# Kernel optimization log

Hardware: AMD Instinct MI355X
Metric: run time of the kernel (lower is better)

The kernel has to match this reference:

```python
import jax, jax.numpy as jnp
from jax import lax
import numpy as np

B, C, T = 128, 9, 512
M = 64                 # fourier modes
D_OB = 40
D_MODEL = C * D_OB     # 360
D_PE = 16
D = D_MODEL + D_PE     # 376
NHEAD = 4
DH = D // NHEAD        # 94
NHID = 2 * D_MODEL     # 720
NLAYERS = 3
FRAC = 0.5
MAX_PE = 100.0
EPS = 1e-5

def setup_inputs() -> dict:
    key = jax.random.key(0)
    ks = jax.random.split(key, 16)
    scale = 1.0 / (C * C)
    f32 = jnp.float32
    return {
        "x": jax.random.normal(ks[0], (B, C, T), f32),
        "w1r": scale * jax.random.uniform(ks[1], (C, C, M), f32),
        "w1i": scale * jax.random.uniform(ks[2], (C, C, M), f32),
        "conv_w": 0.1 * jax.random.normal(ks[3], (1, C, 3), f32),
        "bnf_g": jnp.ones((2 * M,), f32), "bnf_b": jnp.zeros((2 * M,), f32),
        "R_u": 1.0 + 0.02 * jax.random.normal(ks[4], (D_MODEL,), f32),
        "Wg1": 0.1 * jax.random.normal(ks[5], (D_OB, D_OB), f32),
        "Wg2": 0.1 * jax.random.normal(ks[6], (D_OB, D_OB), f32),
        "Wqkv": 0.02 * jax.random.normal(ks[7], (NLAYERS, D, 3 * D), f32),
        "bqkv": jnp.zeros((NLAYERS, 3 * D), f32),
        "Wo": 0.02 * jax.random.normal(ks[8], (NLAYERS, D, D), f32),
        "bo": jnp.zeros((NLAYERS, D), f32),
        "ln1g": jnp.ones((NLAYERS, D), f32), "ln1b": jnp.zeros((NLAYERS, D), f32),
        "W1": 0.02 * jax.random.normal(ks[9], (NLAYERS, D, NHID), f32),
        "b1": jnp.zeros((NLAYERS, NHID), f32),
        "W2": 0.02 * jax.random.normal(ks[10], (NLAYERS, NHID, D), f32),
        "b2": jnp.zeros((NLAYERS, D), f32),
        "ln2g": jnp.ones((NLAYERS, D), f32), "ln2b": jnp.zeros((NLAYERS, D), f32),
        "Wp": 0.02 * jax.random.normal(ks[11], (D, T), f32),
        "bp": jnp.zeros((T,), f32),
        "bnp_g": jnp.ones((T,), f32), "bnp_b": jnp.zeros((T,), f32),
    }

def _layernorm(z, g, b):
    m = z.mean(-1, keepdims=True)
    v = ((z - m) ** 2).mean(-1, keepdims=True)
    return (z - m) * lax.rsqrt(v + EPS) * g + b

def _batchnorm(z, g, b):  # training-mode BN over batch dim, z: [N, F]
    m = z.mean(0)
    v = ((z - m) ** 2).mean(0)
    return (z - m) * lax.rsqrt(v + EPS) * g + b

def _forward(x, w1r, w1i, conv_w, bnf_g, bnf_b, R_u, Wg1, Wg2,
             Wqkv, bqkv, Wo, bo, ln1g, ln1b, W1, b1, W2, b2, ln2g, ln2b,
             Wp, bp, bnp_g, bnp_b):
    # ---- SpectralConv1d (FrFT branch) ----
    xc = jnp.cos(x)                                   # [B,C,T]
    k = jnp.arange(T, dtype=jnp.float32)
    chirp = jnp.exp(-1j * jnp.pi * FRAC * k * k / T)  # FrFT chirp
    x_frft = jnp.fft.ifft(jnp.fft.fft(xc) * chirp)    # [B,C,T] complex
    w1 = (w1r + 1j * w1i).astype(jnp.complex64)
    out_modes = jnp.einsum('bix,iox->box', x_frft[:, :, :M], w1)   # [B,C,M]
    out_ft = jnp.concatenate([out_modes, jnp.zeros((B, C, T - M), jnp.complex64)], -1)
    ef = jnp.concatenate([jnp.abs(out_modes), jnp.angle(out_modes)], -1)  # [B,C,2M]
    # avg: Conv1d(C->1, k=3, pad=1, stride=1, no bias), then squeeze
    ef = lax.conv_general_dilated(ef, conv_w, window_strides=(1,), padding=((1, 1),),
                                  dimension_numbers=('NCH', 'OIH', 'NCH'))[:, 0, :]  # [B,2M]
    ef = jax.nn.relu(_batchnorm(ef, bnf_g, bnf_b))
    # ---- Raindrop branch ----
    src = jnp.transpose(x, (2, 0, 1))                 # [T,B,C]
    h = jnp.repeat(src, D_OB, axis=-1)                # repeat_interleave -> [T,B,d_model]
    h = jax.nn.relu(h * R_u)
    h4 = h.reshape(T, B, C, D_OB)
    adj = jnp.full((C, C), 1.0 / C, x.dtype)          # global_structure = ones, normalized
    h4 = jax.nn.relu(jnp.einsum('mn,tbnd,de->tbme', adj, h4, Wg1))
    h4 = jax.nn.relu(jnp.einsum('mn,tbnd,de->tbme', adj, h4, Wg2))
    h = h4.reshape(T, B, D_MODEL)
    # time positional encoding (PositionalEncodingTF, d_pe=16, MAX=100)
    times = jnp.broadcast_to(jnp.arange(T, dtype=jnp.float32)[:, None], (T, B))
    timescales = jnp.power(MAX_PE, jnp.linspace(0.0, 1.0, D_PE // 2))
    st = times[:, :, None] / timescales               # [T,B,8]
    pe = jnp.concatenate([jnp.sin(st), jnp.cos(st)], -1)  # [T,B,16]
    z = jnp.concatenate([h, pe], -1).transpose(1, 0, 2)   # [B,T,D]
    inv_sqrt_dh = 1.0 / np.sqrt(DH).astype(np.float32)
    for l in range(NLAYERS):
        qkv = z @ Wqkv[l] + bqkv[l]
        q, kk, v = jnp.split(qkv, 3, axis=-1)
        hd = lambda t: t.reshape(B, T, NHEAD, DH).transpose(0, 2, 1, 3)
        q, kk, v = hd(q), hd(kk), hd(v)
        att = jax.nn.softmax(jnp.einsum('bhqd,bhkd->bhqk', q, kk) * inv_sqrt_dh, axis=-1)
        o = jnp.einsum('bhqk,bhkd->bhqd', att, v).transpose(0, 2, 1, 3).reshape(B, T, D)
        z = _layernorm(z + o @ Wo[l] + bo[l], ln1g[l], ln1b[l])
        ff = jax.nn.relu(z @ W1[l] + b1[l]) @ W2[l] + b2[l]
        z = _layernorm(z + ff, ln2g[l], ln2b[l])
    et = z.mean(axis=1)                               # 'mean' aggregation -> [B,D]
    # projection: Linear(D, T) + ReLU + BatchNorm1d(T)
    et = _batchnorm(jax.nn.relu(et @ Wp + bp), bnp_g, bnp_b)  # [B,T]
    f = jnp.concatenate([ef, et], -1)                 # [B, 2M+T]
    fn = f / jnp.maximum(jnp.linalg.norm(f, axis=-1, keepdims=True), 1e-12)
    return fn, out_ft

def reference(x, w1r, w1i, conv_w, bnf_g, bnf_b, R_u, Wg1, Wg2,
              Wqkv, bqkv, Wo, bo, ln1g, ln1b, W1, b1, W2, b2, ln2g, ln2b,
              Wp, bp, bnp_g, bnp_b):
    return _forward(x, w1r, w1i, conv_w, bnf_g, bnf_b, R_u, Wg1, Wg2,
                    Wqkv, bqkv, Wo, bo, ln1g, ln1b, W1, b1, W2, b2, ln2g, ln2b,
                    Wp, bp, bnp_g, bnp_b)
```

## Files before the change

kernel.cpp:

```cpp
#include <hip/hip_runtime.h>
#include <math.h>

constexpr int cB = 128;
constexpr int cC = 9;
constexpr int cT = 512;
constexpr int cM = 64;
constexpr int cDOB = 40;
constexpr int cDM = 360;
constexpr int cD = 376;
constexpr int cDP = 384;
constexpr int cDH = 94;
constexpr int cNHID = 720;
constexpr int cNHP = 736;
constexpr float cEPS = 1e-5f;
constexpr float cPI = 3.14159265358979323846f;

typedef __attribute__((ext_vector_type(8))) short short8b;
typedef __attribute__((ext_vector_type(4))) float f32x4;
typedef const __attribute__((address_space(1))) short glb_short;
typedef __attribute__((address_space(3))) short lds_short;

__device__ __forceinline__ short f2b(float f) {
  union { float f; unsigned u; } c; c.f = f;
  unsigned r = (c.u + 0x7fffu + ((c.u >> 16) & 1u)) >> 16;
  return (short)r;
}
__device__ __forceinline__ float b2f(short h) {
  union { unsigned u; float f; } c; c.u = ((unsigned)(unsigned short)h) << 16;
  return c.f;
}

__global__ void k_chirp(float2* __restrict__ g) {
  int d = threadIdx.x;
  float re = 0.f, im = 0.f;
  for (int k = 0; k < cT; ++k) {
    int q = (k * k) & 2047;
    int p = (k * d) & 511;
    float th = cPI * ((float)p * (1.0f / 256.0f) - (float)q * (1.0f / 1024.0f));
    float s, c;
    sincosf(th, &s, &c);
    re += c; im += s;
  }
  g[d] = make_float2(re * (1.0f / 512.0f), im * (1.0f / 512.0f));
}

__global__ __launch_bounds__(512) void k_spectral(
    const float* __restrict__ x, const float* __restrict__ w1r,
    const float* __restrict__ w1i, const float2* __restrict__ g,
    float* __restrict__ outft, float* __restrict__ EF) {
  __shared__ float xc[cC][cT];
  __shared__ float2 gs[cT];
  __shared__ float2 xfr[cC][cM];
  int b = blockIdx.x, tid = threadIdx.x;
  for (int i = tid; i < cC * cT; i += 512)
    xc[i / cT][i % cT] = cosf(x[(size_t)b * cC * cT + i]);
  for (int i = tid; i < cT; i += 512) gs[i] = g[i];
  __syncthreads();
  for (int idx = tid; idx < cC * cM; idx += 512) {
    int c = idx / cM, m = idx % cM;
    float re = 0.f, im = 0.f;
    for (int t = 0; t < cT; ++t) {
      float xv = xc[c][t];
      float2 gv = gs[(m - t) & (cT - 1)];
      re += xv * gv.x; im += xv * gv.y;
    }
    xfr[c][m] = make_float2(re, im);
  }
  __syncthreads();
  for (int idx = tid; idx < cC * cM; idx += 512) {
    int o = idx / cM, m = idx % cM;
    float re = 0.f, im = 0.f;
    #pragma unroll
    for (int i = 0; i < cC; ++i) {
      float2 xv = xfr[i][m];
      float wr = w1r[(i * cC + o) * cM + m];
      float wi = w1i[(i * cC + o) * cM + m];
      re += xv.x * wr - xv.y * wi;
      im += xv.x * wi + xv.y * wr;
    }
    outft[(size_t)(b * cC + o) * cT + m] = re;
    EF[(b * cC + o) * (2 * cM) + m] = sqrtf(re * re + im * im);
    EF[(b * cC + o) * (2 * cM) + cM + m] = atan2f(im, re);
  }
  for (int idx = tid; idx < cC * (cT - cM); idx += 512) {
    int o = idx / (cT - cM);
    int r = idx % (cT - cM);
    outft[(size_t)(b * cC + o) * cT + cM + r] = 0.f;
  }
}

__global__ void k_convef(const float* __restrict__ EF, const float* __restrict__ cw,
                         float* __restrict__ efp) {
  int i = blockIdx.x * blockDim.x + threadIdx.x;
  if (i >= cB * 2 * cM) return;
  int b = i / (2 * cM), f = i % (2 * cM);
  float acc = 0.f;
  #pragma unroll
  for (int c = 0; c < cC; ++c) {
    const float* row = EF + (b * cC + c) * (2 * cM);
    if (f > 0) acc += row[f - 1] * cw[c * 3 + 0];
    acc += row[f] * cw[c * 3 + 1];
    if (f < 2 * cM - 1) acc += row[f + 1] * cw[c * 3 + 2];
  }
  efp[i] = acc;
}

__global__ __launch_bounds__(128) void k_bn(const float* __restrict__ in,
    const float* __restrict__ gam, const float* __restrict__ bet,
    float* __restrict__ dst, int F, int stride, int off, int reluAfter) {
  __shared__ float red[128];
  int f = blockIdx.x, bt = threadIdx.x;
  float v = in[(size_t)bt * F + f];
  red[bt] = v; __syncthreads();
  for (int s = 64; s > 0; s >>= 1) { if (bt < s) red[bt] += red[bt + s]; __syncthreads(); }
  float mean = red[0] * (1.0f / 128.0f);
  __syncthreads();
  float d = v - mean;
  red[bt] = d * d; __syncthreads();
  for (int s = 64; s > 0; s >>= 1) { if (bt < s) red[bt] += red[bt + s]; __syncthreads(); }
  float var = red[0] * (1.0f / 128.0f);
  float o = d * rsqrtf(var + cEPS) * gam[f] + bet[f];
  if (reluAfter) o = fmaxf(o, 0.f);
  dst[(size_t)bt * stride + off + f] = o;
}

__global__ __launch_bounds__(256) void k_raindrop(const float* __restrict__ x,
    const float* __restrict__ Ru, const float* __restrict__ Wg1,
    const float* __restrict__ Wg2, float* __restrict__ Z,
    short* __restrict__ Zb16, int bStart) {
  __shared__ float w1s[cDOB * cDOB], w2s[cDOB * cDOB], rus[cDM], tss[8];
  __shared__ float vsh[256][cDOB];
  int tid = threadIdx.x;
  for (int i = tid; i < cDOB * cDOB; i += 256) { w1s[i] = Wg1[i]; w2s[i] = Wg2[i]; }
  for (int i = tid; i < cDM; i += 256) rus[i] = Ru[i];
  if (tid < 8) tss[tid] = powf(100.0f, (float)tid * (1.0f / 7.0f));
  __syncthreads();
  int token0 = blockIdx.x * 256;
  int token = token0 + tid;
  int bl = token / cT, t = token % cT;
  int bg = bStart + bl;
  float s[cDOB];
  #pragma unroll
  for (int d = 0; d < cDOB; ++d) s[d] = 0.f;
  #pragma unroll
  for (int c = 0; c < cC; ++c) {
    float xv = x[((size_t)bg * cC + c) * cT + t];
    #pragma unroll
    for (int d = 0; d < cDOB; ++d) s[d] += fmaxf(xv * rus[c * cDOB + d], 0.f);
  }
  #pragma unroll
  for (int d = 0; d < cDOB; ++d) s[d] *= (1.0f / 9.0f);
  float u[cDOB];
  #pragma unroll
  for (int e = 0; e < cDOB; ++e) {
    float a = 0.f;
    #pragma unroll
    for (int d = 0; d < cDOB; ++d) a += s[d] * w1s[d * cDOB + e];
    u[e] = fmaxf(a, 0.f);
  }
  #pragma unroll
  for (int e = 0; e < cDOB; ++e) {
    float a = 0.f;
    #pragma unroll
    for (int d = 0; d < cDOB; ++d) a += u[d] * w2s[d * cDOB + e];
    vsh[tid][e] = fmaxf(a, 0.f);
  }
  __syncthreads();
  size_t zbase = (size_t)token0 * cD;
  for (int i = tid; i < 256 * cD; i += 256) {
    int tok = i / cD, col = i % cD;
    float val;
    if (col < cDM) {
      val = vsh[tok][col % cDOB];
    } else {
      int j = col - cDM;
      int tt = (token0 + tok) % cT;
      float st = (float)tt / tss[j & 7];
      val = (j < 8) ? sinf(st) : cosf(st);
    }
    Z[zbase + i] = val;
    Zb16[(size_t)(token0 + tok) * cDP + col] = f2b(val);
  }
  for (int i = tid; i < 256 * 8; i += 256) {
    int tok = i >> 3, c = cD + (i & 7);
    Zb16[(size_t)(token0 + tok) * cDP + c] = 0;
  }
}

__global__ __launch_bounds__(256) void k_cvtT(const float* __restrict__ in,
    short* __restrict__ out, int K, int N, int Kpad) {
  __shared__ float tile[32][33];
  int kb = blockIdx.x * 32, nb = blockIdx.y * 32;
  int tx = threadIdx.x & 31, ty = threadIdx.x >> 5;
  for (int i = ty; i < 32; i += 8) {
    int k = kb + i, n = nb + tx;
    tile[i][tx] = (k < K && n < N) ? in[(size_t)k * N + n] : 0.f;
  }
  __syncthreads();
  for (int i = ty; i < 32; i += 8) {
    int n = nb + i, k = kb + tx;
    if (n < N && k < Kpad) out[(size_t)n * Kpad + k] = f2b(tile[tx][i]);
  }
}

#define GEMM_CORE(EPILOGUE)                                                       \
  __shared__ __align__(16) short As[128 * 32];                                    \
  __shared__ __align__(16) short Bs[128 * 32];                                    \
  int tid = threadIdx.x;                                                          \
  int nbx = gridDim.x;                                                            \
  int flat = blockIdx.y * nbx + blockIdx.x;                                       \
  int nwg = nbx * gridDim.y;                                                      \
  int swz = ((nwg & 7) == 0) ? ((flat & 7) * (nwg >> 3) + (flat >> 3)) : flat;    \
  int m0 = (swz / nbx) * 128, n0 = (swz % nbx) * 128;                             \
  int w = tid >> 6, l = tid & 63;                                                 \
  int wm = w >> 1, wn = w & 1;                                                    \
  int lr = l & 15, lg = l >> 4;                                                   \
  f32x4 acc[4][4];                                                                \
  _Pragma("unroll") for (int i = 0; i < 4; ++i)                                   \
    _Pragma("unroll") for (int j = 0; j < 4; ++j)                                 \
      _Pragma("unroll") for (int r = 0; r < 4; ++r) acc[i][j][r] = 0.f;           \
  int rbase = w * 32;                                                             \
  int lrow = l >> 2, lslot = l & 3;                                               \
  int nK = Kd >> 5;                                                               \
  for (int ks = 0; ks < nK; ++ks) {                                               \
    int k0 = ks << 5;                                                             \
    _Pragma("unroll") for (int q = 0; q < 2; ++q) {                               \
      int r = rbase + q * 16 + lrow;                                              \
      int cl = lslot ^ ((r >> 1) & 3);                                            \
      __builtin_amdgcn_global_load_lds(                                           \
          (glb_short*)(At + (size_t)(m0 + r) * Kd + k0 + cl * 8),                 \
          (lds_short*)&As[(rbase + q * 16) * 32], 16, 0, 0);                      \
      __builtin_amdgcn_global_load_lds(                                           \
          (glb_short*)(Bt + (size_t)(n0 + r) * Kd + k0 + cl * 8),                 \
          (lds_short*)&Bs[(rbase + q * 16) * 32], 16, 0, 0);                      \
    }                                                                             \
    __syncthreads();                                                              \
    short8b af[4], bf[4];                                                         \
    _Pragma("unroll") for (int i = 0; i < 4; ++i) {                               \
      int row = wm * 64 + i * 16 + lr;                                            \
      int sl = lg ^ ((row >> 1) & 3);                                             \
      af[i] = *(short8b*)&As[row * 32 + sl * 8];                                  \
    }                                                                             \
    _Pragma("unroll") for (int j = 0; j < 4; ++j) {                               \
      int row = wn * 64 + j * 16 + lr;                                            \
      int sl = lg ^ ((row >> 1) & 3);                                             \
      bf[j] = *(short8b*)&Bs[row * 32 + sl * 8];                                  \
    }                                                                             \
    _Pragma("unroll") for (int i = 0; i < 4; ++i)                                 \
      _Pragma("unroll") for (int j = 0; j < 4; ++j)                               \
        acc[i][j] = __builtin_amdgcn_mfma_f32_16x16x32_bf16(af[i], bf[j], acc[i][j], 0, 0, 0); \
    __syncthreads();                                                              \
  }                                                                               \
  _Pragma("unroll") for (int i = 0; i < 4; ++i)                                   \
    _Pragma("unroll") for (int j = 0; j < 4; ++j) {                               \
      int gn = n0 + wn * 64 + j * 16 + lr;                                        \
      if (gn >= Nst) continue;                                                    \
      float bv = (bias && gn < Nc) ? bias[gn] : 0.f;                              \
      int gmb = m0 + wm * 64 + i * 16 + lg * 4;                                   \
      _Pragma("unroll") for (int r = 0; r < 4; ++r) {                             \
        int gm = gmb + r;                                                         \
        if (gm >= Mr) continue;                                                   \
        float vv = acc[i][j][r] + bv;                                             \
        EPILOGUE                                                                  \
      }                                                                           \
    }

__global__ __launch_bounds__(256) void k_gemm_mfma2(
    const short* __restrict__ At, const short* __restrict__ Bt,
    const float* __restrict__ bias, float* __restrict__ Cm,
    int Mr, int Nc, int Nst, int Kd, int relu) {
  GEMM_CORE({
    if (relu) vv = fmaxf(vv, 0.f);
    Cm[(size_t)gm * Nst + gn] = vv;
  })
}

__global__ __launch_bounds__(256) void k_gemm_b16(
    const short* __restrict__ At, const short* __restrict__ Bt,
    const float* __restrict__ bias, short* __restrict__ Cm,
    int Mr, int Nc, int Nst, int Kd, int relu) {
  GEMM_CORE({
    if (relu) vv = fmaxf(vv, 0.f);
    Cm[(size_t)gm * Nst + gn] = (gn < Nc) ? f2b(vv) : (short)0;
  })
}

__global__ __launch_bounds__(256) void k_gemm_qkv(
    const short* __restrict__ At, const short* __restrict__ Bt,
    const float* __restrict__ bias, unsigned* __restrict__ Cp,
    int Mr, int Nc, int Nst, int Kd) {
  GEMM_CORE({
    short hv = f2b(vv);
    short lv2 = f2b(vv - b2f(hv));
    Cp[(size_t)gm * Nst + gn] =
        ((unsigned)(unsigned short)hv) | (((unsigned)(unsigned short)lv2) << 16);
  })
}

__global__ __launch_bounds__(256) void k_gemm(const float* __restrict__ A,
    const float* __restrict__ Bm, const float* __restrict__ bias,
    float* __restrict__ Cm, int Mr, int Nc, int Kd, int relu) {
  __shared__ float As[16][68];
  __shared__ float Bs[16][68];
  int tid = threadIdx.x;
  int tx = tid & 15, ty = tid >> 4;
  int n0 = blockIdx.x * 64, m0 = blockIdx.y * 64;
  float acc[4][4] = {{0.f}};
  for (int k0 = 0; k0 < Kd; k0 += 16) {
    {
      int row = tid >> 2, kq = (tid & 3) << 2;
      int gm = m0 + row, gk = k0 + kq;
      float4 av = make_float4(0.f, 0.f, 0.f, 0.f);
      if (gm < Mr) {
        const float* ap = A + (size_t)gm * Kd + gk;
        if (gk + 3 < Kd) av = *(const float4*)ap;
        else {
          if (gk + 0 < Kd) av.x = ap[0];
          if (gk + 1 < Kd) av.y = ap[1];
          if (gk + 2 < Kd) av.z = ap[2];
        }
      }
      As[kq + 0][row] = av.x; As[kq + 1][row] = av.y;
      As[kq + 2][row] = av.z; As[kq + 3][row] = av.w;
    }
    {
      int kr = tid >> 4, nc = (tid & 15) << 2;
      int gk = k0 + kr, gn = n0 + nc;
      float4 bv = make_float4(0.f, 0.f, 0.f, 0.f);
      if (gk < Kd && gn < Nc) {
        const float* bp = Bm + (size_t)gk * Nc + gn;
        if (gn + 3 < Nc) bv = *(const float4*)bp;
        else {
          bv.x = bp[0];
          if (gn + 1 < Nc) bv.y = bp[1];
          if (gn + 2 < Nc) bv.z = bp[2];
        }
      }
      *(float4*)&Bs[kr][nc] = bv;
    }
    __syncthreads();
    #pragma unroll
    for (int k = 0; k < 16; ++k) {
      float4 a = *(const float4*)&As[k][ty << 2];
      float4 b = *(const float4*)&Bs[k][tx << 2];
      acc[0][0] += a.x * b.x; acc[0][1] += a.x * b.y; acc[0][2] += a.x * b.z; acc[0][3] += a.x * b.w;
      acc[1][0] += a.y * b.x; acc[1][1] += a.y * b.y; acc[1][2] += a.y * b.z; acc[1][3] += a.y * b.w;
      acc[2][0] += a.z * b.x; acc[2][1] += a.z * b.y; acc[2][2] += a.z * b.z; acc[2][3] += a.z * b.w;
      acc[3][0] += a.w * b.x; acc[3][1] += a.w * b.y; acc[3][2] += a.w * b.z; acc[3][3] += a.w * b.w;
    }
    __syncthreads();
  }
  #pragma unroll
  for (int i = 0; i < 4; ++i) {
    int gm = m0 + (ty << 2) + i;
    if (gm >= Mr) continue;
    #pragma unroll
    for (int j = 0; j < 4; ++j) {
      int gn = n0 + (tx << 2) + j;
      if (gn >= Nc) continue;
      float v = acc[i][j] + (bias ? bias[gn] : 0.f);
      if (relu) v = fmaxf(v, 0.f);
      Cm[(size_t)gm * Nc + gn] = v;
    }
  }
}

__global__ __launch_bounds__(512) void k_attn_mfma2(const unsigned* __restrict__ Qp,
    short* __restrict__ ATT16) {
  __shared__ __align__(16) char raw[62464];
  short* kv_h = (short*)raw;
  short* kv_l = (short*)(raw + 12288);
  int tid = threadIdx.x;
  int w = tid >> 6, l = tid & 63;
  int lr = l & 15, lg = l >> 4;
  short* p_h = (short*)(raw + 24576) + w * 16 * 72;
  short* p_l = (short*)(raw + 43008) + w * 16 * 72;
  float* fs_w = (float*)(raw + 61440) + w * 16;
  float* il_w = (float*)(raw + 61952) + w * 16;
  int qb = blockIdx.x, h = blockIdx.y, bl = blockIdx.z;
  size_t tokBase = (size_t)bl * cT;
  const float scale = 0.103142125f;
  int qrow = w * 16 + lr;

  short8b qh_s[3], ql_s[3];
  #pragma unroll
  for (int ph = 0; ph < 2; ++ph) {
    size_t base = (tokBase + qb * 128 + ph * 64) * 1128ull + h * cDH;
    for (int task = tid; task < 768; task += 512) {
      int oct = task >> 6, tok = task & 63;
      size_t src = base + (size_t)tok * 1128 + oct * 8;
      uint4 a = *(const uint4*)(Qp + src);
      uint4 b = *(const uint4*)(Qp + src + 4);
      unsigned p[8] = {a.x, a.y, a.z, a.w, b.x, b.y, b.z, b.w};
      short hv[8], lv[8];
      #pragma unroll
      for (int i = 0; i < 8; ++i) { hv[i] = (short)(p[i] & 0xffffu); lv[i] = (short)(p[i] >> 16); }
      if (oct == 11) { hv[6] = 0; hv[7] = 0; lv[6] = 0; lv[7] = 0; }
      int dst = (oct * 64 + (tok ^ (oct & 7))) * 8;
      *(short8b*)&kv_h[dst] = *(short8b*)hv;
      *(short8b*)&kv_l[dst] = *(short8b*)lv;
    }
    __syncthreads();
    if ((w >> 2) == ph) {
      int tokl = qrow & 63;
      #pragma unroll
      for (int s = 0; s < 3; ++s) {
        int o = s * 4 + lg;
        int src = (o * 64 + (tokl ^ (o & 7))) * 8;
        qh_s[s] = *(short8b*)&kv_h[src];
        ql_s[s] = *(short8b*)&kv_l[src];
      }
    }
    __syncthreads();
  }

  f32x4 of[6];
  #pragma unroll
  for (int f = 0; f < 6; ++f)
    #pragma unroll
    for (int r = 0; r < 4; ++r) of[f][r] = 0.f;
  float mrow[4], lrow[4];
  #pragma unroll
  for (int r = 0; r < 4; ++r) { mrow[r] = -1e30f; lrow[r] = 0.f; }

  for (int kt = 0; kt < 8; ++kt) {
    __syncthreads();
    {
      size_t base = (tokBase + kt * 64) * 1128ull + cD + h * cDH;
      for (int task = tid; task < 768; task += 512) {
        int oct = task >> 6, tok = task & 63;
        size_t src = base + (size_t)tok * 1128 + oct * 8;
        uint4 a = *(const uint4*)(Qp + src);
        uint4 b = *(const uint4*)(Qp + src + 4);
        unsigned p[8] = {a.x, a.y, a.z, a.w, b.x, b.y, b.z, b.w};
        short hv[8], lv[8];
        #pragma unroll
        for (int i = 0; i < 8; ++i) { hv[i] = (short)(p[i] & 0xffffu); lv[i] = (short)(p[i] >> 16); }
        if (oct == 11) { hv[6] = 0; hv[7] = 0; lv[6] = 0; lv[7] = 0; }
        int dst = (oct * 64 + (tok ^ (oct & 7))) * 8;
        *(short8b*)&kv_h[dst] = *(short8b*)hv;
        *(short8b*)&kv_l[dst] = *(short8b*)lv;
      }
    }
    __syncthreads();
    f32x4 sf4[4];
    #pragma unroll
    for (int j = 0; j < 4; ++j)
      #pragma unroll
      for (int r = 0; r < 4; ++r) sf4[j][r] = 0.f;
    #pragma unroll
    for (int j = 0; j < 4; ++j) {
      #pragma unroll
      for (int s = 0; s < 3; ++s) {
        int o = s * 4 + lg;
        int src = (o * 64 + ((j * 16 + lr) ^ (o & 7))) * 8;
        short8b bh = *(short8b*)&kv_h[src];
        short8b bl2 = *(short8b*)&kv_l[src];
        sf4[j] = __builtin_amdgcn_mfma_f32_16x16x32_bf16(qh_s[s], bh, sf4[j], 0, 0, 0);
        sf4[j] = __builtin_amdgcn_mfma_f32_16x16x32_bf16(ql_s[s], bh, sf4[j], 0, 0, 0);
        sf4[j] = __builtin_amdgcn_mfma_f32_16x16x32_bf16(qh_s[s], bl2, sf4[j], 0, 0, 0);
      }
    }
    float fscv[4];
    #pragma unroll
    for (int r = 0; r < 4; ++r) {
      float s0 = sf4[0][r] * scale, s1 = sf4[1][r] * scale;
      float s2 = sf4[2][r] * scale, s3 = sf4[3][r] * scale;
      float mx = fmaxf(fmaxf(s0, s1), fmaxf(s2, s3));
      for (int off = 8; off > 0; off >>= 1) mx = fmaxf(mx, __shfl_xor(mx, off, 16));
      float mnew = fmaxf(mrow[r], mx);
      float fsc = __expf(mrow[r] - mnew);
      float p0 = __expf(s0 - mnew), p1 = __expf(s1 - mnew);
      float p2 = __expf(s2 - mnew), p3 = __expf(s3 - mnew);
      float ps = p0 + p1 + p2 + p3;
      for (int off = 8; off > 0; off >>= 1) ps += __shfl_xor(ps, off, 16);
      lrow[r] = lrow[r] * fsc + ps;
      mrow[r] = mnew;
      fscv[r] = fsc;
      int row = (lg * 4 + r) * 72;
      short h0 = f2b(p0);
      p_h[row + 0 * 16 + lr] = h0; p_l[row + 0 * 16 + lr] = f2b(p0 - b2f(h0));
      short h1 = f2b(p1);
      p_h[row + 1 * 16 + lr] = h1; p_l[row + 1 * 16 + lr] = f2b(p1 - b2f(h1));
      short h2 = f2b(p2);
      p_h[row + 2 * 16 + lr] = h2; p_l[row + 2 * 16 + lr] = f2b(p2 - b2f(h2));
      short h3 = f2b(p3);
      p_h[row + 3 * 16 + lr] = h3; p_l[row + 3 * 16 + lr] = f2b(p3 - b2f(h3));
    }
    if (lr == 0) {
      #pragma unroll
      for (int r = 0; r < 4; ++r) fs_w[lg * 4 + r] = fscv[r];
    }
    __syncthreads();
    {
      size_t base = (tokBase + kt * 64) * 1128ull + 2 * cD + h * cDH;
      for (int task = tid; task < 768; task += 512) {
        int d = task % 96, t8 = task / 96;
        short hv[8], lv[8];
        if (d < cDH) {
          #pragma unroll
          for (int i = 0; i < 8; ++i) {
            unsigned p = Qp[base + (size_t)(t8 * 8 + i) * 1128 + d];
            hv[i] = (short)(p & 0xffffu); lv[i] = (short)(p >> 16);
          }
        } else {
          #pragma unroll
          for (int i = 0; i < 8; ++i) { hv[i] = 0; lv[i] = 0; }
        }
        int dst = d * 64 + ((t8 * 8) ^ ((d & 7) << 3));
        *(short8b*)&kv_h[dst] = *(short8b*)hv;
        *(short8b*)&kv_l[dst] = *(short8b*)lv;
      }
    }
    __syncthreads();
    float fs = fs_w[lr];
    #pragma unroll
    for (int f = 0; f < 6; ++f)
      #pragma unroll
      for (int r = 0; r < 4; ++r) of[f][r] *= fs;
    #pragma unroll
    for (int s = 0; s < 2; ++s) {
      int pof = lr * 72 + s * 32 + lg * 8;
      short8b ph = *(short8b*)&p_h[pof];
      short8b pl = *(short8b*)&p_l[pof];
      #pragma unroll
      for (int f = 0; f < 6; ++f) {
        int d = f * 16 + lr;
        int vof = d * 64 + ((s * 32 + lg * 8) ^ ((d & 7) << 3));
        short8b vh = *(short8b*)&kv_h[vof];
        short8b vl = *(short8b*)&kv_l[vof];
        of[f] = __builtin_amdgcn_mfma_f32_16x16x32_bf16(vh, ph, of[f], 0, 0, 0);
        of[f] = __builtin_amdgcn_mfma_f32_16x16x32_bf16(vl, ph, of[f], 0, 0, 0);
        of[f] = __builtin_amdgcn_mfma_f32_16x16x32_bf16(vh, pl, of[f], 0, 0, 0);
      }
    }
  }
  if (lr == 0) {
    #pragma unroll
    for (int r = 0; r < 4; ++r) il_w[lg * 4 + r] = 1.0f / lrow[r];
  }
  __syncthreads();
  float il = il_w[lr];
  float* obuf = (float*)raw;
  #pragma unroll
  for (int f = 0; f < 6; ++f) {
    #pragma unroll
    for (int r = 0; r < 4; ++r) {
      int d = f * 16 + lg * 4 + r;
      if (d < cDH) obuf[(w * 16 + lr) * 98 + d] = of[f][r] * il;
    }
  }
  __syncthreads();
  for (int idx = tid; idx < 128 * cDH; idx += 512) {
    int q = idx / cDH, d = idx % cDH;
    ATT16[(tokBase + qb * 128 + q) * (size_t)cDP + h * cDH + d] = f2b(obuf[q * 98 + d]);
  }
  if (h == 3) {
    for (int idx = tid; idx < 128 * 8; idx += 512) {
      int q = idx >> 3, c = cD + (idx & 7);
      ATT16[(tokBase + qb * 128 + q) * (size_t)cDP + c] = 0;
    }
  }
}

__global__ __launch_bounds__(256) void k_addln(float* __restrict__ Z,
    const float* __restrict__ Y, const float* __restrict__ gam,
    const float* __restrict__ bet, short* __restrict__ Zb16) {
  int wid = threadIdx.x >> 6, lane = threadIdx.x & 63;
  size_t token = (size_t)blockIdx.x * 4 + wid;
  size_t base = token * cD;
  size_t b16 = token * cDP;
  float v[6];
  float sum = 0.f;
  #pragma unroll
  for (int j = 0; j < 6; ++j) {
    int c = lane + j * 64;
    float t = 0.f;
    if (c < cD) t = Z[base + c] + Y[base + c];
    v[j] = t; sum += t;
  }
  #pragma unroll
  for (int off = 32; off > 0; off >>= 1) sum += __shfl_xor(sum, off, 64);
  float mean = sum / (float)cD;
  float vs = 0.f;
  #pragma unroll
  for (int j = 0; j < 6; ++j) {
    int c = lane + j * 64;
    if (c < cD) { float d = v[j] - mean; vs += d * d; }
  }
  #pragma unroll
  for (int off = 32; off > 0; off >>= 1) vs += __shfl_xor(vs, off, 64);
  float inv = rsqrtf(vs / (float)cD + cEPS);
  #pragma unroll
  for (int j = 0; j < 6; ++j) {
    int c = lane + j * 64;
    if (c < cD) {
      float res = (v[j] - mean) * inv * gam[c] + bet[c];
      Z[base + c] = res;
      Zb16[b16 + c] = f2b(res);
    } else if (c < cDP) {
      Zb16[b16 + c] = 0;
    }
  }
}

__global__ __launch_bounds__(384) void k_meant(const float* __restrict__ Z,
    float* __restrict__ et, int bStart) {
  int bl = blockIdx.x, d = threadIdx.x;
  if (d >= cD) return;
  float s = 0.f;
  for (int t = 0; t < cT; ++t) s += Z[((size_t)bl * cT + t) * cD + d];
  et[(size_t)(bStart + bl) * cD + d] = s * (1.0f / 512.0f);
}

__global__ __launch_bounds__(128) void k_final(const float* __restrict__ fst,
    float* __restrict__ out) {
  __shared__ float red[128];
  int b = blockIdx.x, tid = threadIdx.x;
  float v[5]; float ss = 0.f;
  #pragma unroll
  for (int i = 0; i < 5; ++i) {
    v[i] = fst[(size_t)b * 640 + tid + i * 128];
    ss += v[i] * v[i];
  }
  red[tid] = ss; __syncthreads();
  for (int s = 64; s > 0; s >>= 1) { if (tid < s) red[tid] += red[tid + s]; __syncthreads(); }
  float inv = 1.0f / fmaxf(sqrtf(red[0]), 1e-12f);
  #pragma unroll
  for (int i = 0; i < 5; ++i) out[(size_t)b * 640 + tid + i * 128] = v[i] * inv;
}

extern "C" void kernel_launch(void* const* d_in, const int* in_sizes, int n_in,
                              void* d_out, int out_size, void* d_ws, size_t ws_size,
                              hipStream_t stream) {
  (void)in_sizes; (void)n_in; (void)out_size;
  const float* x     = (const float*)d_in[0];
  const float* w1r   = (const float*)d_in[1];
  const float* w1i   = (const float*)d_in[2];
  const float* convw = (const float*)d_in[3];
  const float* bnfg  = (const float*)d_in[4];
  const float* bnfb  = (const float*)d_in[5];
  const float* Ru    = (const float*)d_in[6];
  const float* Wg1   = (const float*)d_in[7];
  const float* Wg2   = (const float*)d_in[8];
  const float* Wqkv  = (const float*)d_in[9];
  const float* bqkv  = (const float*)d_in[10];
  const float* Wo    = (const float*)d_in[11];
  const float* bo    = (const float*)d_in[12];
  const float* ln1g  = (const float*)d_in[13];
  const float* ln1b  = (const float*)d_in[14];
  const float* W1    = (const float*)d_in[15];
  const float* b1    = (const float*)d_in[16];
  const float* W2    = (const float*)d_in[17];
  const float* b2    = (const float*)d_in[18];
  const float* ln2g  = (const float*)d_in[19];
  const float* ln2b  = (const float*)d_in[20];
  const float* Wp    = (const float*)d_in[21];
  const float* bp    = (const float*)d_in[22];
  const float* bnpg  = (const float*)d_in[23];
  const float* bnpb  = (const float*)d_in[24];

  float* W = (float*)d_ws;
  size_t wsFloats = ws_size / 4;
  float* fst = W;
  float* et  = fst + 81920;
  float* etp = et + 48128;
  float2* g  = (float2*)(etp + 65536);
  float* EF  = (float*)g + 1024;
  float* efp = EF + 147456;
  short* bfw = (short*)(efp + 16384);
  const size_t oQKV = 0;
  const size_t oWO  = oQKV + (size_t)3 * 1128 * cDP;
  const size_t oW1  = oWO  + (size_t)3 * 376 * cDP;
  const size_t oW2  = oW1  + (size_t)3 * 720 * cDP;
  const size_t bfwShorts = oW2 + (size_t)3 * 376 * cNHP;
  const size_t bfwFloats = (bfwShorts + 1) / 2;
  const size_t fixedFloats = 81920 + 48128 + 65536 + 1024 + 147456 + 16384 + bfwFloats;

  float* outF  = (float*)d_out;
  float* outft = outF + cB * 640;

  if (wsFloats < fixedFloats) return;

  int Bc = 0;
  float* chunk = nullptr;
  for (int c = 128; c >= 1; c >>= 1) {
    size_t need = (size_t)c * cT * 1888 + 64;
    if (fixedFloats + need <= wsFloats) { Bc = c; chunk = W + fixedFloats; break; }
  }
  bool haveChunk = (Bc > 0);

  if (haveChunk) {
    for (int l = 0; l < 3; ++l) {
      k_cvtT<<<dim3(12, 36), 256, 0, stream>>>(Wqkv + (size_t)l * cD * 1128,
          bfw + oQKV + (size_t)l * 1128 * cDP, cD, 1128, cDP);
      k_cvtT<<<dim3(12, 12), 256, 0, stream>>>(Wo + (size_t)l * cD * cD,
          bfw + oWO + (size_t)l * 376 * cDP, cD, cD, cDP);
      k_cvtT<<<dim3(12, 23), 256, 0, stream>>>(W1 + (size_t)l * cD * cNHID,
          bfw + oW1 + (size_t)l * 720 * cDP, cD, cNHID, cDP);
      k_cvtT<<<dim3(23, 12), 256, 0, stream>>>(W2 + (size_t)l * cNHID * cD,
          bfw + oW2 + (size_t)l * 376 * cNHP, cNHID, cD, cNHP);
    }

    float* Zb      = chunk;
    short* Zb16    = (short*)(Zb + (size_t)Bc * cT * cD);
    unsigned* QKVp = (unsigned*)(Zb16 + (size_t)Bc * cT * cDP);
    short* ATT16   = (short*)(QKVp + (size_t)Bc * cT * 1128);
    for (int b0 = 0; b0 < cB; b0 += Bc) {
      int ntok = Bc * cT;
      int mt = (ntok + 127) / 128;
      short* Hb16  = (short*)QKVp;
      float* WoOut = (float*)(Hb16 + (size_t)ntok * cNHP);
      float* FF2o  = WoOut + (size_t)ntok * 376;
      k_raindrop<<<ntok / 256, 256, 0, stream>>>(x, Ru, Wg1, Wg2, Zb, Zb16, b0);
      for (int l = 0; l < 3; ++l) {
        k_gemm_qkv<<<dim3(9, mt), 256, 0, stream>>>(
            Zb16, bfw + oQKV + (size_t)l * 1128 * cDP,
            bqkv + (size_t)l * 1128, QKVp, ntok, 1128, 1128, cDP);
        k_attn_mfma2<<<dim3(4, 4, Bc), 512, 0, stream>>>(QKVp, ATT16);
        k_gemm_mfma2<<<dim3(3, mt), 256, 0, stream>>>(
            ATT16, bfw + oWO + (size_t)l * 376 * cDP,
            bo + (size_t)l * cD, WoOut, ntok, cD, cD, cDP, 0);
        k_addln<<<ntok / 4, 256, 0, stream>>>(Zb, WoOut, ln1g + l * cD, ln1b + l * cD, Zb16);
        k_gemm_b16<<<dim3(6, mt), 256, 0, stream>>>(
            Zb16, bfw + oW1 + (size_t)l * 720 * cDP,
            b1 + (size_t)l * cNHID, Hb16, ntok, cNHID, cNHP, cDP, 1);
        k_gemm_mfma2<<<dim3(3, mt), 256, 0, stream>>>(
            Hb16, bfw + oW2 + (size_t)l * 376 * cNHP,
            b2 + (size_t)l * cD, FF2o, ntok, cD, cD, cNHP, 0);
        k_addln<<<ntok / 4, 256, 0, stream>>>(Zb, FF2o, ln2g + l * cD, ln2b + l * cD, Zb16);
      }
      k_meant<<<Bc, 384, 0, stream>>>(Zb, et, b0);
    }
    k_gemm<<<dim3(cT / 64, cB / 64), 256, 0, stream>>>(et, Wp, bp, etp, cB, cT, cD, 1);
  }

  k_chirp<<<1, 512, 0, stream>>>(g);
  k_spectral<<<cB, 512, 0, stream>>>(x, w1r, w1i, g, outft, EF);
  k_convef<<<(cB * 2 * cM + 255) / 256, 256, 0, stream>>>(EF, convw, efp);
  k_bn<<<2 * cM, 128, 0, stream>>>(efp, bnfg, bnfb, fst, 2 * cM, 640, 0, 1);

  if (haveChunk)
    k_bn<<<cT, 128, 0, stream>>>(etp, bnpg, bnpb, fst, cT, 640, 2 * cM, 0);

  k_final<<<cB, 128, 0, stream>>>(fst, outF);
}
```

Before: 2.651 ms.

## Fuse Wo and FF2 GEMMs with residual add and LayerNorm

Replaces the separate output-projection and FF2 GEMMs plus the add+LayerNorm kernels with one kernel, where each 512-thread block owns 128 full rows (all 384 padded columns). The row mean and variance are reduced in-kernel through shuffles and a small shared buffer. This removes the fp32 intermediate write and reread and two launches per layer. In exchange the grid shrinks to one block per 128 rows, which lowers parallelism, and each block holds more accumulator registers. The B-weight buffer is padded so the 384-row tile load of the 376-row weights does not read out of bounds.

```diff
diff --git a/kernel.cpp b/kernel.cpp
--- a/kernel.cpp
+++ b/kernel.cpp
@@ -265,16 +265,6 @@
       }                                                                           \
     }
 
-__global__ __launch_bounds__(256) void k_gemm_mfma2(
-    const short* __restrict__ At, const short* __restrict__ Bt,
-    const float* __restrict__ bias, float* __restrict__ Cm,
-    int Mr, int Nc, int Nst, int Kd, int relu) {
-  GEMM_CORE({
-    if (relu) vv = fmaxf(vv, 0.f);
-    Cm[(size_t)gm * Nst + gn] = vv;
-  })
-}
-
 __global__ __launch_bounds__(256) void k_gemm_b16(
     const short* __restrict__ At, const short* __restrict__ Bt,
     const float* __restrict__ bias, short* __restrict__ Cm,
@@ -295,6 +285,185 @@
     Cp[(size_t)gm * Nst + gn] =
         ((unsigned)(unsigned short)hv) | (((unsigned)(unsigned short)lv2) << 16);
   })
+}
+
+__global__ __launch_bounds__(512) void k_gemm_ln(
+    const short* __restrict__ At, const short* __restrict__ Bt,
+    const float* __restrict__ bias, const float* __restrict__ gam,
+    const float* __restrict__ bet, float* __restrict__ Z,
+    short* __restrict__ Zb16, int Mr, int Kd) {
+  __shared__ __align__(16) short As[128 * 32];
+  __shared__ __align__(16) short Bs[384 * 32];
+  __shared__ float red[128][4];
+  int tid = threadIdx.x;
+  int nwg = gridDim.x;
+  int flat = blockIdx.x;
+  int swz = ((nwg & 7) == 0) ? ((flat & 7) * (nwg >> 3) + (flat >> 3)) : flat;
+  int m0 = swz * 128;
+  int w = tid >> 6, l = tid & 63;
+  int wm = w >> 2, wn = w & 3;
+  int lr = l & 15, lg = l >> 4;
+  f32x4 acc[4][6];
+  #pragma unroll
+  for (int i = 0; i < 4; ++i)
+    #pragma unroll
+    for (int j = 0; j < 6; ++j)
+      #pragma unroll
+      for (int r = 0; r < 4; ++r) acc[i][j][r] = 0.f;
+  int lrow = l >> 2, lslot = l & 3;
+  int nK = Kd >> 5;
+  for (int ks = 0; ks < nK; ++ks) {
+    int k0 = ks << 5;
+    {
+      int r = w * 16 + lrow;
+      int cl = lslot ^ ((r >> 1) & 3);
+      __builtin_amdgcn_global_load_lds(
+          (glb_short*)(At + (size_t)(m0 + r) * Kd + k0 + cl * 8),
+          (lds_short*)&As[(w * 16) * 32], 16, 0, 0);
+    }
+    #pragma unroll
+    for (int q = 0; q < 3; ++q) {
+      int r = q * 128 + w * 16 + lrow;
+      int cl = lslot ^ ((r >> 1) & 3);
+      __builtin_amdgcn_global_load_lds(
+          (glb_short*)(Bt + (size_t)r * Kd + k0 + cl * 8),
+          (lds_short*)&Bs[(q * 128 + w * 16) * 32], 16, 0, 0);
+    }
+    __syncthreads();
+    short8b af[4], bf[6];
+    #pragma unroll
+    for (int i = 0; i < 4; ++i) {
+      int row = wm * 64 + i * 16 + lr;
+      int sl = lg ^ ((row >> 1) & 3);
+      af[i] = *(short8b*)&As[row * 32 + sl * 8];
+    }
+    #pragma unroll
+    for (int j = 0; j < 6; ++j) {
+      int row = wn * 96 + j * 16 + lr;
+      int sl = lg ^ ((row >> 1) & 3);
+      bf[j] = *(short8b*)&Bs[row * 32 + sl * 8];
+    }
+    #pragma unroll
+    for (int i = 0; i < 4; ++i)
+      #pragma unroll
+      for (int j = 0; j < 6; ++j)
+        acc[i][j] = __builtin_amdgcn_mfma_f32_16x16x32_bf16(af[i], bf[j], acc[i][j], 0, 0, 0);
+    __syncthreads();
+  }
+  int gnj[6]; float bvj[6], gamj[6], betj[6]; bool vcj[6];
+  #pragma unroll
+  for (int j = 0; j < 6; ++j) {
+    int gn = wn * 96 + j * 16 + lr;
+    gnj[j] = gn;
+    vcj[j] = (gn < cD);
+    bvj[j] = vcj[j] ? bias[gn] : 0.f;
+    gamj[j] = vcj[j] ? gam[gn] : 0.f;
+    betj[j] = vcj[j] ? bet[gn] : 0.f;
+  }
+  float ps[4][4];
+  #pragma unroll
+  for (int i = 0; i < 4; ++i)
+    #pragma unroll
+    for (int r = 0; r < 4; ++r) ps[i][r] = 0.f;
+  #pragma unroll
+  for (int i = 0; i < 4; ++i)
+    #pragma unroll
+    for (int r = 0; r < 4; ++r) {
+      int gm = m0 + wm * 64 + i * 16 + lg * 4 + r;
+      if (gm >= Mr) continue;
+      float s = 0.f;
+      #pragma unroll
+      for (int j = 0; j < 6; ++j)
+        if (vcj[j]) s += acc[i][j][r] + bvj[j] + Z[(size_t)gm * cD + gnj[j]];
+      ps[i][r] = s;
+    }
+  #pragma unroll
+  for (int i = 0; i < 4; ++i)
+    #pragma unroll
+    for (int r = 0; r < 4; ++r) {
+      float s = ps[i][r];
+      #pragma unroll
+      for (int off = 8; off > 0; off >>= 1) s += __shfl_xor(s, off, 16);
+      ps[i][r] = s;
+    }
+  if (lr == 0) {
+    #pragma unroll
+    for (int i = 0; i < 4; ++i)
+      #pragma unroll
+      for (int r = 0; r < 4; ++r)
+        red[wm * 64 + i * 16 + lg * 4 + r][wn] = ps[i][r];
+  }
+  __syncthreads();
+  float mean[4][4];
+  #pragma unroll
+  for (int i = 0; i < 4; ++i)
+    #pragma unroll
+    for (int r = 0; r < 4; ++r) {
+      int lw = wm * 64 + i * 16 + lg * 4 + r;
+      mean[i][r] = (red[lw][0] + red[lw][1] + red[lw][2] + red[lw][3]) / (float)cD;
+    }
+  __syncthreads();
+  #pragma unroll
+  for (int i = 0; i < 4; ++i)
+    #pragma unroll
+    for (int r = 0; r < 4; ++r) {
+      int gm = m0 + wm * 64 + i * 16 + lg * 4 + r;
+      float s = 0.f;
+      if (gm < Mr) {
+        #pragma unroll
+        for (int j = 0; j < 6; ++j)
+          if (vcj[j]) {
+            float t = acc[i][j][r] + bvj[j] + Z[(size_t)gm * cD + gnj[j]] - mean[i][r];
+            s += t * t;
+          }
+      }
+      ps[i][r] = s;
+    }
+  #pragma unroll
+  for (int i = 0; i < 4; ++i)
+    #pragma unroll
+    for (int r = 0; r < 4; ++r) {
+      float s = ps[i][r];
+      #pragma unroll
+      for (int off = 8; off > 0; off >>= 1) s += __shfl_xor(s, off, 16);
+      ps[i][r] = s;
+    }
+  if (lr == 0) {
+    #pragma unroll
+    for (int i = 0; i < 4; ++i)
+      #pragma unroll
+      for (int r = 0; r < 4; ++r)
+        red[wm * 64 + i * 16 + lg * 4 + r][wn] = ps[i][r];
+  }
+  __syncthreads();
+  float inv[4][4];
+  #pragma unroll
+  for (int i = 0; i < 4; ++i)
+    #pragma unroll
+    for (int r = 0; r < 4; ++r) {
+      int lw = wm * 64 + i * 16 + lg * 4 + r;
+      float v = (red[lw][0] + red[lw][1] + red[lw][2] + red[lw][3]) / (float)cD;
+      inv[i][r] = rsqrtf(v + cEPS);
+    }
+  #pragma unroll
+  for (int i = 0; i < 4; ++i)
+    #pragma unroll
+    for (int r = 0; r < 4; ++r) {
+      int gm = m0 + wm * 64 + i * 16 + lg * 4 + r;
+      if (gm >= Mr) continue;
+      #pragma unroll
+      for (int j = 0; j < 6; ++j) {
+        int gn = gnj[j];
+        if (vcj[j]) {
+          float t = acc[i][j][r] + bvj[j] + Z[(size_t)gm * cD + gn];
+          float res = (t - mean[i][r]) * inv[i][r] * gamj[j] + betj[j];
+          Z[(size_t)gm * cD + gn] = res;
+          Zb16[(size_t)gm * cDP + gn] = f2b(res);
+        } else if (gn < cDP) {
+          Zb16[(size_t)gm * cDP + gn] = 0;
+        }
+      }
+    }
 }
 
 __global__ __launch_bounds__(256) void k_gemm(const float* __restrict__ A,
@@ -559,47 +728,6 @@
     for (int idx = tid; idx < 128 * 8; idx += 512) {
       int q = idx >> 3, c = cD + (idx & 7);
       ATT16[(tokBase + qb * 128 + q) * (size_t)cDP + c] = 0;
-    }
-  }
-}
-
-__global__ __launch_bounds__(256) void k_addln(float* __restrict__ Z,
-    const float* __restrict__ Y, const float* __restrict__ gam,
-    const float* __restrict__ bet, short* __restrict__ Zb16) {
-  int wid = threadIdx.x >> 6, lane = threadIdx.x & 63;
-  size_t token = (size_t)blockIdx.x * 4 + wid;
-  size_t base = token * cD;
-  size_t b16 = token * cDP;
-  float v[6];
-  float sum = 0.f;
-  #pragma unroll
-  for (int j = 0; j < 6; ++j) {
-    int c = lane + j * 64;
-    float t = 0.f;
-    if (c < cD) t = Z[base + c] + Y[base + c];
-    v[j] = t; sum += t;
-  }
-  #pragma unroll
-  for (int off = 32; off > 0; off >>= 1) sum += __shfl_xor(sum, off, 64);
-  float mean = sum / (float)cD;
-  float vs = 0.f;
-  #pragma unroll
-  for (int j = 0; j < 6; ++j) {
-    int c = lane + j * 64;
-    if (c < cD) { float d = v[j] - mean; vs += d * d; }
-  }
-  #pragma unroll
-  for (int off = 32; off > 0; off >>= 1) vs += __shfl_xor(vs, off, 64);
-  float inv = rsqrtf(vs / (float)cD + cEPS);
-  #pragma unroll
-  for (int j = 0; j < 6; ++j) {
-    int c = lane + j * 64;
-    if (c < cD) {
-      float res = (v[j] - mean) * inv * gam[c] + bet[c];
-      Z[base + c] = res;
-      Zb16[b16 + c] = f2b(res);
-    } else if (c < cDP) {
-      Zb16[b16 + c] = 0;
     }
   }
 }
@@ -673,7 +801,7 @@
   const size_t oWO  = oQKV + (size_t)3 * 1128 * cDP;
   const size_t oW1  = oWO  + (size_t)3 * 376 * cDP;
   const size_t oW2  = oW1  + (size_t)3 * 720 * cDP;
-  const size_t bfwShorts = oW2 + (size_t)3 * 376 * cNHP;
+  const size_t bfwShorts = oW2 + (size_t)3 * 376 * cNHP + 1024;
   const size_t bfwFloats = (bfwShorts + 1) / 2;
   const size_t fixedFloats = 81920 + 48128 + 65536 + 1024 + 147456 + 16384 + bfwFloats;
 
@@ -709,26 +837,24 @@
     for (int b0 = 0; b0 < cB; b0 += Bc) {
       int ntok = Bc * cT;
       int mt = (ntok + 127) / 128;
-      short* Hb16  = (short*)QKVp;
-      float* WoOut = (float*)(Hb16 + (size_t)ntok * cNHP);
-      float* FF2o  = WoOut + (size_t)ntok * 376;
+      short* Hb16 = (short*)QKVp;
       k_raindrop<<<ntok / 256, 256, 0, stream>>>(x, Ru, Wg1, Wg2, Zb, Zb16, b0);
       for (int l = 0; l < 3; ++l) {
         k_gemm_qkv<<<dim3(9, mt), 256, 0, stream>>>(
             Zb16, bfw + oQKV + (size_t)l * 1128 * cDP,
             bqkv + (size_t)l * 1128, QKVp, ntok, 1128, 1128, cDP);
         k_attn_mfma2<<<dim3(4, 4, Bc), 512, 0, stream>>>(QKVp, ATT16);
-        k_gemm_mfma2<<<dim3(3, mt), 256, 0, stream>>>(
+        k_gemm_ln<<<mt, 512, 0, stream>>>(
             ATT16, bfw + oWO + (size_t)l * 376 * cDP,
-            bo + (size_t)l * cD, WoOut, ntok, cD, cD, cDP, 0);
-        k_addln<<<ntok / 4, 256, 0, stream>>>(Zb, WoOut, ln1g + l * cD, ln1b + l * cD, Zb16);
+            bo + (size_t)l * cD, ln1g + l * cD, ln1b + l * cD,
+            Zb, Zb16, ntok, cDP);
         k_gemm_b16<<<dim3(6, mt), 256, 0, stream>>>(
             Zb16, bfw + oW1 + (size_t)l * 720 * cDP,
             b1 + (size_t)l * cNHID, Hb16, ntok, cNHID, cNHP, cDP, 1);
-        k_gemm_mfma2<<<dim3(3, mt), 256, 0, stream>>>(
+        k_gemm_ln<<<mt, 512, 0, stream>>>(
             Hb16, bfw + oW2 + (size_t)l * 376 * cNHP,
-            b2 + (size_t)l * cD, FF2o, ntok, cD, cD, cNHP, 0);
-        k_addln<<<ntok / 4, 256, 0, stream>>>(Zb, FF2o, ln2g + l * cD, ln2b + l * cD, Zb16);
+            b2 + (size_t)l * cD, ln2g + l * cD, ln2b + l * cD,
+            Zb, Zb16, ntok, cNHP);
       }
       k_meant<<<Bc, 384, 0, stream>>>(Zb, et, b0);
     }
```

New measurement: 2.749 ms. 3.7% more time.
